# Performance work log

Hardware: AMD Instinct MI355X
Metric: run time of the kernel (lower is better)

The kernel has to match this reference:

```python
import jax, jax.numpy as jnp
import numpy as np

FEA_DIM = 256
NUM_HEADS = 8
B, N = 32, 48


def setup_inputs() -> dict:
    key = jax.random.key(0)
    ks = jax.random.split(key, 30)
    d = FEA_DIM
    inp = {
        "async_fea": jax.random.normal(ks[0], (B, N, d), dtype=jnp.float32),
        "sync_fea": jax.random.normal(ks[1], (B, N, d), dtype=jnp.float32),
        "async_adj": jax.random.randint(ks[2], (B, N, N), 0, 2, dtype=jnp.int32),
        "sync_adj": jax.random.randint(ks[3], (B, N, N), 0, 2, dtype=jnp.int32),
    }
    i = 4
    for pref in ("a_", "s_"):
        for nm in ("Wq", "Wk", "Wv", "Wo", "Wm"):
            inp[pref + nm] = 0.02 * jax.random.normal(ks[i], (d, d), dtype=jnp.float32); i += 1
            inp[pref + nm.replace("W", "b")] = 0.02 * jax.random.normal(ks[i], (d,), dtype=jnp.float32); i += 1
    return inp


def _aggregate(x_src, adj, fallback, Wq, bq, Wk, bk, Wv, bv, Wo, bo, Wm, bm):
    """For each target t: self-attention among neighbor set {s : adj[b,s,t] > 0}
    of x_src, mean-pool over neighbors, divide by count again, linear map.
    Targets with no neighbors fall back to `fallback`."""
    Bb, Nn, D = x_src.shape
    H = NUM_HEADS
    dh = D // H
    q = (x_src @ Wq.T + bq).reshape(Bb, Nn, H, dh)
    k = (x_src @ Wk.T + bk).reshape(Bb, Nn, H, dh)
    v = (x_src @ Wv.T + bv).reshape(Bb, Nn, H, dh)
    # shared pairwise scores among source nodes: [B, H, Q, K]
    scores = jnp.einsum("bqhd,bkhd->bhqk", q, k) / jnp.sqrt(jnp.float32(dh))
    # neighbor mask per target: adj[b, s, t] > 0 -> m[b, t, s]
    m = jnp.transpose(adj > 0, (0, 2, 1))  # [B, T, S] bool
    # per-target masked softmax over keys: logits [B, T, H, Q, K]
    key_bias = jnp.where(m[:, :, None, None, :], 0.0, -1e9)
    attn = jax.nn.softmax(scores[:, None] + key_bias, axis=-1)  # [B,T,H,Q,K]
    out = jnp.einsum("bthqk,bkhd->bthqd", attn, v).reshape(Bb, Nn, Nn, D)  # [B,T,Q,D]
    out = out @ Wo.T + bo
    mf = m.astype(out.dtype)  # [B, T, Q]
    cnt = mf.sum(-1)  # [B, T]
    denom = jnp.maximum(cnt, 1.0)
    # torch: mean over valid queries, then / edge_cnt  => sum / cnt^2
    pooled = jnp.einsum("btq,btqd->btd", mf, out) / (denom * denom)[..., None]
    mapped = pooled @ Wm.T + bm
    return jnp.where((cnt > 0)[..., None], mapped, fallback)


def reference(async_fea, sync_fea, async_adj, sync_adj,
              a_Wq, a_bq, a_Wk, a_bk, a_Wv, a_bv, a_Wo, a_bo, a_Wm, a_bm,
              s_Wq, s_bq, s_Wk, s_bk, s_Wv, s_bv, s_Wo, s_bo, s_Wm, s_bm):
    refined_async = _aggregate(sync_fea, sync_adj, async_fea,
                               a_Wq, a_bq, a_Wk, a_bk, a_Wv, a_bv, a_Wo, a_bo, a_Wm, a_bm)
    refined_sync = _aggregate(async_fea, async_adj, sync_fea,
                              s_Wq, s_bq, s_Wk, s_bk, s_Wv, s_bv, s_Wo, s_bo, s_Wm, s_bm)
    return jnp.concatenate([refined_async, refined_sync, async_fea, sync_fea], axis=2)
```

## Files before the change

### kernel.cpp

```cpp
#include <hip/hip_runtime.h>

typedef __attribute__((ext_vector_type(8))) short short8v;
typedef __attribute__((ext_vector_type(4))) float f32x4;

#define XPAD 264
#define ESTR 52

__device__ __forceinline__ unsigned short f2bf(float f) {
    union { float f; unsigned u; } v; v.f = f;
    unsigned u = v.u;
    return (unsigned short)((u + 0x7FFFu + ((u >> 16) & 1u)) >> 16);
}
__device__ __forceinline__ float bf2f(unsigned short u) {
    union { unsigned u; float f; } v; v.u = ((unsigned)u) << 16; return v.f;
}
__device__ __forceinline__ short8v cvt8(const float* p) {
    float4 lo = *(const float4*)p;
    float4 hi = *(const float4*)(p + 4);
    union { uint4 u; short8v s; } r;
    asm("v_cvt_pk_bf16_f32 %0, %1, %2" : "=v"(r.u.x) : "v"(lo.x), "v"(lo.y));
    asm("v_cvt_pk_bf16_f32 %0, %1, %2" : "=v"(r.u.y) : "v"(lo.z), "v"(lo.w));
    asm("v_cvt_pk_bf16_f32 %0, %1, %2" : "=v"(r.u.z) : "v"(hi.x), "v"(hi.y));
    asm("v_cvt_pk_bf16_f32 %0, %1, %2" : "=v"(r.u.w) : "v"(hi.z), "v"(hi.w));
    return r.s;
}

struct AggParams {
    const float *async_fea, *sync_fea;
    const int *async_adj, *sync_adj;
    const float *aWq, *abq, *aWk, *abk, *aWv, *abv, *aWo, *abo, *aWm, *abm;
    const float *sWq, *sbq, *sWk, *sbk, *sWv, *sbv, *sWo, *sbo, *sWm, *sbm;
    float *out;
};

__global__ __launch_bounds__(512) void block_kernel(AggParams p)
{
    __shared__ __attribute__((aligned(16))) char sm[118336];
    unsigned short* E_l  = (unsigned short*)(sm);
    unsigned short* Xb   = (unsigned short*)(sm);
    unsigned short* Qb   = (unsigned short*)(sm + 39936);
    float*          invd = (float*)(sm + 39936);
    unsigned short* Kb   = (unsigned short*)(sm + 65280);
    unsigned short* yv   = (unsigned short*)(sm + 65280);
    unsigned short* P_l  = (unsigned short*)(sm + 74592);
    unsigned short* Vb   = (unsigned short*)(sm + 90624);
    unsigned short* pool_l = (unsigned short*)(sm + 90624);
    float* msk   = (float*)(sm + 115968);
    float* cnt_l = (float*)(sm + 118272);

    const int bid = blockIdx.x, tid = threadIdx.x;
    const int agg = bid >> 7, rem = bid & 127;
    const int b = rem >> 2, tg = rem & 3;
    const int wave = tid >> 6, lane = tid & 63;
    const int l15 = lane & 15, g = lane >> 4;
    const int row_base = b * 48 + tg * 12;

    const float* Xsrc = agg ? p.async_fea : p.sync_fea;
    const float* fb   = agg ? p.sync_fea  : p.async_fea;
    const int*   adj  = agg ? p.async_adj : p.sync_adj;

    #pragma unroll
    for (int l = 0; l < 3; ++l) {
        int idx = l * 4096 + tid * 8;
        int row = idx >> 8, col = idx & 255;
        short8v v = cvt8(Xsrc + (b * 48 + row) * 256 + col);
        *(short8v*)(Xb + row * XPAD + col) = v;
    }
    for (int e = tid; e < 576; e += 512) {
        int tt = e / 48, s = e % 48;
        msk[tt * 48 + s] = (adj[(b * 48 + s) * 48 + tg * 12 + tt] > 0) ? 1.f : 0.f;
    }
    {
        const float4* fb4 = (const float4*)fb;
        float4* out4 = (float4*)p.out;
        for (int e = tid; e < 768; e += 512) {
            int r = e >> 6, c = e & 63;
            out4[(row_base + r) * 256 + 128 + agg * 64 + c] =
                fb4[(row_base + r) * 64 + c];
        }
    }
    __syncthreads();
    if (tid < 12) {
        float c = 0.f;
        for (int s = 0; s < 48; ++s) c += msk[tid * 48 + s];
        cnt_l[tid] = c;
    }

    for (int job = wave; job < 48; job += 8) {
        int mat = job >> 4;
        int cm = (job & 15) * 16;
        const float* W; const float* bias;
        if (agg == 0) {
            W    = (mat == 0) ? p.aWq : (mat == 1) ? p.aWk : p.aWv;
            bias = (mat == 0) ? p.abq : (mat == 1) ? p.abk : p.abv;
        } else {
            W    = (mat == 0) ? p.sWq : (mat == 1) ? p.sWk : p.sWv;
            bias = (mat == 0) ? p.sbq : (mat == 1) ? p.sbk : p.sbv;
        }
        const float* Wp = W + (cm + l15) * 256 + g * 8;
        f32x4 acc[3] = {{0,0,0,0},{0,0,0,0},{0,0,0,0}};
        #pragma unroll
        for (int kk = 0; kk < 8; ++kk) {
            short8v bf = cvt8(Wp + kk * 32);
            #pragma unroll
            for (int rt = 0; rt < 3; ++rt) {
                short8v a = *(const short8v*)(Xb + (rt * 16 + l15) * XPAD + kk * 32 + g * 8);
                acc[rt] = __builtin_amdgcn_mfma_f32_16x16x32_bf16(a, bf, acc[rt], 0, 0, 0);
            }
        }
        float bv = bias[cm + l15];
        unsigned short* dst = (mat == 0) ? Qb : (mat == 1) ? Kb : Vb;
        #pragma unroll
        for (int rt = 0; rt < 3; ++rt)
            #pragma unroll
            for (int i = 0; i < 4; ++i) {
                int row = rt * 16 + g * 4 + i;
                dst[row * XPAD + cm + l15] = f2bf(acc[rt][i] + bv);
            }
    }
    __syncthreads();

    const float scale = 0.17677669529663687f;
    #pragma unroll
    for (int jj = 0; jj < 3; ++jj) {
        int job = wave * 3 + jj;
        int h = job / 3, qt = job % 3;
        short8v a = *(const short8v*)(Qb + (qt * 16 + l15) * XPAD + h * 32 + g * 8);
        f32x4 acc[3];
        #pragma unroll
        for (int kt = 0; kt < 3; ++kt) {
            short8v kb = *(const short8v*)(Kb + (kt * 16 + l15) * XPAD + h * 32 + g * 8);
            f32x4 z = {0.f, 0.f, 0.f, 0.f};
            acc[kt] = __builtin_amdgcn_mfma_f32_16x16x32_bf16(a, kb, z, 0, 0, 0);
        }
        float sc[3][4], rm[4];
        #pragma unroll
        for (int i = 0; i < 4; ++i) {
            #pragma unroll
            for (int kt = 0; kt < 3; ++kt) sc[kt][i] = acc[kt][i] * scale;
            rm[i] = fmaxf(fmaxf(sc[0][i], sc[1][i]), sc[2][i]);
        }
        #pragma unroll
        for (int m = 1; m <= 8; m <<= 1)
            #pragma unroll
            for (int i = 0; i < 4; ++i) rm[i] = fmaxf(rm[i], __shfl_xor(rm[i], m));
        #pragma unroll
        for (int kt = 0; kt < 3; ++kt)
            #pragma unroll
            for (int i = 0; i < 4; ++i)
                E_l[(h * 48 + qt * 16 + g * 4 + i) * ESTR + kt * 16 + l15] =
                    f2bf(__expf(sc[kt][i] - rm[i]));
    }
    __syncthreads();

    if (tid < 384) {
        float erow[48];
        const uint2* er = (const uint2*)(E_l + tid * ESTR);
        #pragma unroll
        for (int v = 0; v < 12; ++v) {
            uint2 u = er[v];
            erow[v * 4 + 0] = bf2f((unsigned short)(u.x & 0xFFFF));
            erow[v * 4 + 1] = bf2f((unsigned short)(u.x >> 16));
            erow[v * 4 + 2] = bf2f((unsigned short)(u.y & 0xFFFF));
            erow[v * 4 + 3] = bf2f((unsigned short)(u.y >> 16));
        }
        int q = tid % 48;
        #pragma unroll
        for (int tt = 0; tt < 12; ++tt) {
            const float4* m4p = (const float4*)&msk[tt * 48];
            float ss = 0.f;
            #pragma unroll
            for (int k4 = 0; k4 < 12; ++k4) {
                float4 m4 = m4p[k4];
                ss += m4.x * erow[4 * k4] + m4.y * erow[4 * k4 + 1]
                    + m4.z * erow[4 * k4 + 2] + m4.w * erow[4 * k4 + 3];
            }
            invd[tt * 384 + tid] = (msk[tt * 48 + q] > 0.f) ? (1.f / ss) : 0.f;
        }
    }
    __syncthreads();

    if (tid < 384) {
        int h2 = tid / 48, k = tid % 48;
        float ecol[48];
        #pragma unroll
        for (int q = 0; q < 48; ++q) ecol[q] = bf2f(E_l[(h2 * 48 + q) * ESTR + k]);
        #pragma unroll
        for (int tt = 0; tt < 12; ++tt) {
            const float4* iv4 = (const float4*)&invd[tt * 384 + h2 * 48];
            float ss = 0.f;
            #pragma unroll
            for (int q4 = 0; q4 < 12; ++q4) {
                float4 v = iv4[q4];
                ss += v.x * ecol[4 * q4] + v.y * ecol[4 * q4 + 1]
                    + v.z * ecol[4 * q4 + 2] + v.w * ecol[4 * q4 + 3];
            }
            yv[tt * 388 + tid] = f2bf(msk[tt * 48 + k] * ss);
        }
    }
    __syncthreads();

    for (int e = tid; e < 1024; e += 512) {
        if (e < 768) {
            int tt = e >> 6, d4 = e & 63;
            const unsigned short* yr = yv + tt * 388 + (d4 >> 3) * 48;
            float px = 0.f, py = 0.f, pz = 0.f, pw = 0.f;
            #pragma unroll
            for (int k = 0; k < 48; ++k) {
                float yval = bf2f(yr[k]);
                uint2 vv = *(const uint2*)(Vb + k * XPAD + d4 * 4);
                px += yval * bf2f((unsigned short)(vv.x & 0xFFFF));
                py += yval * bf2f((unsigned short)(vv.x >> 16));
                pz += yval * bf2f((unsigned short)(vv.y & 0xFFFF));
                pw += yval * bf2f((unsigned short)(vv.y >> 16));
            }
            uint2 pk;
            pk.x = (unsigned)f2bf(px) | ((unsigned)f2bf(py) << 16);
            pk.y = (unsigned)f2bf(pz) | ((unsigned)f2bf(pw) << 16);
            *(uint2*)(P_l + tt * 264 + d4 * 4) = pk;
        } else {
            int e2 = e - 768;
            int tt = 12 + (e2 >> 6), d4 = e2 & 63;
            uint2 z; z.x = 0u; z.y = 0u;
            *(uint2*)(P_l + tt * 264 + d4 * 4) = z;
        }
    }
    __syncthreads();

    {
        const float* Wo = agg ? p.sWo : p.aWo;
        const float* bo = agg ? p.sbo : p.abo;
        for (int ct = wave; ct < 16; ct += 8) {
            f32x4 acc = {0.f, 0.f, 0.f, 0.f};
            const float* Wp = Wo + (ct * 16 + l15) * 256 + g * 8;
            #pragma unroll
            for (int kk = 0; kk < 8; ++kk) {
                short8v a = *(const short8v*)(P_l + l15 * 264 + kk * 32 + g * 8);
                short8v bf = cvt8(Wp + kk * 32);
                acc = __builtin_amdgcn_mfma_f32_16x16x32_bf16(a, bf, acc, 0, 0, 0);
            }
            int c = ct * 16 + l15;
            float bov = bo[c];
            #pragma unroll
            for (int i = 0; i < 4; ++i) {
                int t = g * 4 + i;
                float val = 0.f;
                if (t < 12) {
                    float cn = cnt_l[t];
                    float i1 = (cn > 0.f) ? 1.f / cn : 0.f;
                    val = acc[i] * i1 * i1 + bov * i1;
                }
                pool_l[t * 264 + c] = f2bf(val);
            }
        }
    }
    __syncthreads();

    {
        const float* Wm = agg ? p.sWm : p.aWm;
        const float* bm = agg ? p.sbm : p.abm;
        for (int ct = wave; ct < 16; ct += 8) {
            f32x4 acc = {0.f, 0.f, 0.f, 0.f};
            const float* Wp = Wm + (ct * 16 + l15) * 256 + g * 8;
            #pragma unroll
            for (int kk = 0; kk < 8; ++kk) {
                short8v a = *(const short8v*)(pool_l + l15 * 264 + kk * 32 + g * 8);
                short8v bf = cvt8(Wp + kk * 32);
                acc = __builtin_amdgcn_mfma_f32_16x16x32_bf16(a, bf, acc, 0, 0, 0);
            }
            int c = ct * 16 + l15;
            float bmv = bm[c];
            #pragma unroll
            for (int i = 0; i < 4; ++i) {
                int t = g * 4 + i;
                if (t < 12) {
                    int grow = row_base + t;
                    float cn = cnt_l[t];
                    float val = (cn > 0.f) ? (acc[i] + bmv) : fb[grow * 256 + c];
                    p.out[grow * 1024 + agg * 256 + c] = val;
                }
            }
        }
    }
}

extern "C" void kernel_launch(void* const* d_in, const int* in_sizes, int n_in,
                              void* d_out, int out_size, void* d_ws, size_t ws_size,
                              hipStream_t stream)
{
    AggParams p;
    p.async_fea = (const float*)d_in[0];
    p.sync_fea  = (const float*)d_in[1];
    p.async_adj = (const int*)d_in[2];
    p.sync_adj  = (const int*)d_in[3];
    p.aWq = (const float*)d_in[4];   p.abq = (const float*)d_in[5];
    p.aWk = (const float*)d_in[6];   p.abk = (const float*)d_in[7];
    p.aWv = (const float*)d_in[8];   p.abv = (const float*)d_in[9];
    p.aWo = (const float*)d_in[10];  p.abo = (const float*)d_in[11];
    p.aWm = (const float*)d_in[12];  p.abm = (const float*)d_in[13];
    p.sWq = (const float*)d_in[14];  p.sbq = (const float*)d_in[15];
    p.sWk = (const float*)d_in[16];  p.sbk = (const float*)d_in[17];
    p.sWv = (const float*)d_in[18];  p.sbv = (const float*)d_in[19];
    p.sWo = (const float*)d_in[20];  p.sbo = (const float*)d_in[21];
    p.sWm = (const float*)d_in[22];  p.sbm = (const float*)d_in[23];
    p.out = (float*)d_out;

    block_kernel<<<256, 512, 0, stream>>>(p);
}
```

Baseline: 60.00 us.

## Move masked-softmax denominators and attention pooling onto bf16 MFMA

Replaces the three scalar stages (per-target softmax denominators, inverse-weighted column sums, and the y·V pooling) with small 16x16x32 bf16 MFMA tiles. To support this it stores E both row-major and transposed, keeps V transposed, and packs the mask as bf16 with padded stride. The goal is to cut the long scalar FMA loops and the per-thread register arrays. In exchange it uses more LDS (about 159KB), which lowers occupancy, and it adds bf16 rounding to the mask-weighted sums.

```diff
diff --git a/kernel.cpp b/kernel.cpp
--- a/kernel.cpp
+++ b/kernel.cpp
@@ -2,16 +2,31 @@
 
 typedef __attribute__((ext_vector_type(8))) short short8v;
 typedef __attribute__((ext_vector_type(4))) float f32x4;
-
-#define XPAD 264
-#define ESTR 52
-
-__device__ __forceinline__ unsigned short f2bf(float f) {
+typedef unsigned short u16t;
+
+#define XP 264
+#define SP 52
+
+#define E_OFF    0
+#define ET_OFF   39936
+#define QB_OFF   79872
+#define KB_OFF   105216
+#define VT_OFF   130560
+#define MSK_OFF  157184
+#define CNT_OFF  158848
+#define SM_SIZE  158912
+#define XB_OFF   E_OFF
+#define IV_OFF   QB_OFF
+#define PL_OFF   (QB_OFF + 13312)
+#define YV_OFF   KB_OFF
+#define PO_OFF   (KB_OFF + 13312)
+
+__device__ __forceinline__ u16t f2bf(float f) {
     union { float f; unsigned u; } v; v.f = f;
     unsigned u = v.u;
-    return (unsigned short)((u + 0x7FFFu + ((u >> 16) & 1u)) >> 16);
-}
-__device__ __forceinline__ float bf2f(unsigned short u) {
+    return (u16t)((u + 0x7FFFu + ((u >> 16) & 1u)) >> 16);
+}
+__device__ __forceinline__ float bf2f(u16t u) {
     union { unsigned u; float f; } v; v.u = ((unsigned)u) << 16; return v.f;
 }
 __device__ __forceinline__ short8v cvt8(const float* p) {
@@ -24,6 +39,12 @@
     asm("v_cvt_pk_bf16_f32 %0, %1, %2" : "=v"(r.u.w) : "v"(hi.z), "v"(hi.w));
     return r.s;
 }
+__device__ __forceinline__ short8v ld52(const u16t* p) {
+    union { uint2 u[2]; short8v s; } r;
+    r.u[0] = *(const uint2*)(p);
+    r.u[1] = *(const uint2*)(p + 4);
+    return r.s;
+}
 
 struct AggParams {
     const float *async_fea, *sync_fea;
@@ -35,18 +56,19 @@
 
 __global__ __launch_bounds__(512) void block_kernel(AggParams p)
 {
-    __shared__ __attribute__((aligned(16))) char sm[118336];
-    unsigned short* E_l  = (unsigned short*)(sm);
-    unsigned short* Xb   = (unsigned short*)(sm);
-    unsigned short* Qb   = (unsigned short*)(sm + 39936);
-    float*          invd = (float*)(sm + 39936);
-    unsigned short* Kb   = (unsigned short*)(sm + 65280);
-    unsigned short* yv   = (unsigned short*)(sm + 65280);
-    unsigned short* P_l  = (unsigned short*)(sm + 74592);
-    unsigned short* Vb   = (unsigned short*)(sm + 90624);
-    unsigned short* pool_l = (unsigned short*)(sm + 90624);
-    float* msk   = (float*)(sm + 115968);
-    float* cnt_l = (float*)(sm + 118272);
+    __shared__ __attribute__((aligned(16))) char sm[SM_SIZE];
+    u16t* E_   = (u16t*)(sm + E_OFF);
+    u16t* ET_  = (u16t*)(sm + ET_OFF);
+    u16t* Xb   = (u16t*)(sm + XB_OFF);
+    u16t* Qb   = (u16t*)(sm + QB_OFF);
+    u16t* Kb   = (u16t*)(sm + KB_OFF);
+    u16t* VT   = (u16t*)(sm + VT_OFF);
+    u16t* mskb = (u16t*)(sm + MSK_OFF);
+    u16t* iv_  = (u16t*)(sm + IV_OFF);
+    u16t* yv_  = (u16t*)(sm + YV_OFF);
+    u16t* P_l  = (u16t*)(sm + PL_OFF);
+    u16t* po_  = (u16t*)(sm + PO_OFF);
+    float* cnt_l = (float*)(sm + CNT_OFF);
 
     const int bid = blockIdx.x, tid = threadIdx.x;
     const int agg = bid >> 7, rem = bid & 127;
@@ -63,12 +85,14 @@
     for (int l = 0; l < 3; ++l) {
         int idx = l * 4096 + tid * 8;
         int row = idx >> 8, col = idx & 255;
-        short8v v = cvt8(Xsrc + (b * 48 + row) * 256 + col);
-        *(short8v*)(Xb + row * XPAD + col) = v;
-    }
-    for (int e = tid; e < 576; e += 512) {
-        int tt = e / 48, s = e % 48;
-        msk[tt * 48 + s] = (adj[(b * 48 + s) * 48 + tg * 12 + tt] > 0) ? 1.f : 0.f;
+        *(short8v*)(Xb + row * XP + col) = cvt8(Xsrc + (b * 48 + row) * 256 + col);
+    }
+    for (int e = tid; e < 16 * SP; e += 512) {
+        int tt = e / SP, k = e - tt * SP;
+        u16t v = 0;
+        if (tt < 12 && k < 48)
+            v = (adj[(b * 48 + k) * 48 + tg * 12 + tt] > 0) ? (u16t)0x3F80 : (u16t)0;
+        mskb[e] = v;
     }
     {
         const float4* fb4 = (const float4*)fb;
@@ -82,7 +106,7 @@
     __syncthreads();
     if (tid < 12) {
         float c = 0.f;
-        for (int s = 0; s < 48; ++s) c += msk[tid * 48 + s];
+        for (int s = 0; s < 48; ++s) c += bf2f(mskb[tid * SP + s]);
         cnt_l[tid] = c;
     }
 
@@ -104,19 +128,25 @@
             short8v bf = cvt8(Wp + kk * 32);
             #pragma unroll
             for (int rt = 0; rt < 3; ++rt) {
-                short8v a = *(const short8v*)(Xb + (rt * 16 + l15) * XPAD + kk * 32 + g * 8);
+                short8v a = *(const short8v*)(Xb + (rt * 16 + l15) * XP + kk * 32 + g * 8);
                 acc[rt] = __builtin_amdgcn_mfma_f32_16x16x32_bf16(a, bf, acc[rt], 0, 0, 0);
             }
         }
         float bv = bias[cm + l15];
-        unsigned short* dst = (mat == 0) ? Qb : (mat == 1) ? Kb : Vb;
-        #pragma unroll
-        for (int rt = 0; rt < 3; ++rt)
-            #pragma unroll
-            for (int i = 0; i < 4; ++i) {
-                int row = rt * 16 + g * 4 + i;
-                dst[row * XPAD + cm + l15] = f2bf(acc[rt][i] + bv);
-            }
+        if (mat < 2) {
+            u16t* dst = (mat == 0) ? Qb : Kb;
+            #pragma unroll
+            for (int rt = 0; rt < 3; ++rt)
+                #pragma unroll
+                for (int i = 0; i < 4; ++i)
+                    dst[(rt * 16 + g * 4 + i) * XP + cm + l15] = f2bf(acc[rt][i] + bv);
+        } else {
+            #pragma unroll
+            for (int rt = 0; rt < 3; ++rt)
+                #pragma unroll
+                for (int i = 0; i < 4; ++i)
+                    VT[(cm + l15) * SP + rt * 16 + g * 4 + i] = f2bf(acc[rt][i] + bv);
+        }
     }
     __syncthreads();
 
@@ -125,11 +155,11 @@
     for (int jj = 0; jj < 3; ++jj) {
         int job = wave * 3 + jj;
         int h = job / 3, qt = job % 3;
-        short8v a = *(const short8v*)(Qb + (qt * 16 + l15) * XPAD + h * 32 + g * 8);
+        short8v a = *(const short8v*)(Qb + (qt * 16 + l15) * XP + h * 32 + g * 8);
         f32x4 acc[3];
         #pragma unroll
         for (int kt = 0; kt < 3; ++kt) {
-            short8v kb = *(const short8v*)(Kb + (kt * 16 + l15) * XPAD + h * 32 + g * 8);
+            short8v kb = *(const short8v*)(Kb + (kt * 16 + l15) * XP + h * 32 + g * 8);
             f32x4 z = {0.f, 0.f, 0.f, 0.f};
             acc[kt] = __builtin_amdgcn_mfma_f32_16x16x32_bf16(a, kb, z, 0, 0, 0);
         }
@@ -147,95 +177,87 @@
         #pragma unroll
         for (int kt = 0; kt < 3; ++kt)
             #pragma unroll
-            for (int i = 0; i < 4; ++i)
-                E_l[(h * 48 + qt * 16 + g * 4 + i) * ESTR + kt * 16 + l15] =
-                    f2bf(__expf(sc[kt][i] - rm[i]));
-    }
-    __syncthreads();
-
-    if (tid < 384) {
-        float erow[48];
-        const uint2* er = (const uint2*)(E_l + tid * ESTR);
-        #pragma unroll
-        for (int v = 0; v < 12; ++v) {
-            uint2 u = er[v];
-            erow[v * 4 + 0] = bf2f((unsigned short)(u.x & 0xFFFF));
-            erow[v * 4 + 1] = bf2f((unsigned short)(u.x >> 16));
-            erow[v * 4 + 2] = bf2f((unsigned short)(u.y & 0xFFFF));
-            erow[v * 4 + 3] = bf2f((unsigned short)(u.y >> 16));
-        }
-        int q = tid % 48;
-        #pragma unroll
-        for (int tt = 0; tt < 12; ++tt) {
-            const float4* m4p = (const float4*)&msk[tt * 48];
-            float ss = 0.f;
-            #pragma unroll
-            for (int k4 = 0; k4 < 12; ++k4) {
-                float4 m4 = m4p[k4];
-                ss += m4.x * erow[4 * k4] + m4.y * erow[4 * k4 + 1]
-                    + m4.z * erow[4 * k4 + 2] + m4.w * erow[4 * k4 + 3];
-            }
-            invd[tt * 384 + tid] = (msk[tt * 48 + q] > 0.f) ? (1.f / ss) : 0.f;
-        }
-    }
-    __syncthreads();
-
-    if (tid < 384) {
-        int h2 = tid / 48, k = tid % 48;
-        float ecol[48];
-        #pragma unroll
-        for (int q = 0; q < 48; ++q) ecol[q] = bf2f(E_l[(h2 * 48 + q) * ESTR + k]);
-        #pragma unroll
-        for (int tt = 0; tt < 12; ++tt) {
-            const float4* iv4 = (const float4*)&invd[tt * 384 + h2 * 48];
-            float ss = 0.f;
-            #pragma unroll
-            for (int q4 = 0; q4 < 12; ++q4) {
-                float4 v = iv4[q4];
-                ss += v.x * ecol[4 * q4] + v.y * ecol[4 * q4 + 1]
-                    + v.z * ecol[4 * q4 + 2] + v.w * ecol[4 * q4 + 3];
-            }
-            yv[tt * 388 + tid] = f2bf(msk[tt * 48 + k] * ss);
-        }
-    }
-    __syncthreads();
-
-    for (int e = tid; e < 1024; e += 512) {
-        if (e < 768) {
-            int tt = e >> 6, d4 = e & 63;
-            const unsigned short* yr = yv + tt * 388 + (d4 >> 3) * 48;
-            float px = 0.f, py = 0.f, pz = 0.f, pw = 0.f;
-            #pragma unroll
-            for (int k = 0; k < 48; ++k) {
-                float yval = bf2f(yr[k]);
-                uint2 vv = *(const uint2*)(Vb + k * XPAD + d4 * 4);
-                px += yval * bf2f((unsigned short)(vv.x & 0xFFFF));
-                py += yval * bf2f((unsigned short)(vv.x >> 16));
-                pz += yval * bf2f((unsigned short)(vv.y & 0xFFFF));
-                pw += yval * bf2f((unsigned short)(vv.y >> 16));
-            }
-            uint2 pk;
-            pk.x = (unsigned)f2bf(px) | ((unsigned)f2bf(py) << 16);
-            pk.y = (unsigned)f2bf(pz) | ((unsigned)f2bf(pw) << 16);
-            *(uint2*)(P_l + tt * 264 + d4 * 4) = pk;
-        } else {
-            int e2 = e - 768;
-            int tt = 12 + (e2 >> 6), d4 = e2 & 63;
-            uint2 z; z.x = 0u; z.y = 0u;
-            *(uint2*)(P_l + tt * 264 + d4 * 4) = z;
-        }
+            for (int i = 0; i < 4; ++i) {
+                u16t ev = f2bf(__expf(sc[kt][i] - rm[i]));
+                int q = qt * 16 + g * 4 + i, k = kt * 16 + l15;
+                E_[(h * 48 + q) * SP + k] = ev;
+                ET_[(h * 48 + k) * SP + q] = ev;
+            }
+    }
+    __syncthreads();
+
+    #pragma unroll
+    for (int jj = 0; jj < 3; ++jj) {
+        int rt = wave * 3 + jj;
+        const u16t* Arow = E_ + (rt * 16 + l15) * SP;
+        const u16t* Brow = mskb + l15 * SP;
+        f32x4 acc = {0.f, 0.f, 0.f, 0.f};
+        short8v a0 = ld52(Arow + g * 8), b0 = ld52(Brow + g * 8);
+        acc = __builtin_amdgcn_mfma_f32_16x16x32_bf16(a0, b0, acc, 0, 0, 0);
+        short8v a1 = {0,0,0,0,0,0,0,0}, b1 = {0,0,0,0,0,0,0,0};
+        if (g < 2) { a1 = ld52(Arow + 32 + g * 8); b1 = ld52(Brow + 32 + g * 8); }
+        acc = __builtin_amdgcn_mfma_f32_16x16x32_bf16(a1, b1, acc, 0, 0, 0);
+        #pragma unroll
+        for (int i = 0; i < 4; ++i) {
+            int row = rt * 16 + g * 4 + i;
+            int h = row / 48, q = row - h * 48;
+            float mq = bf2f(mskb[l15 * SP + q]);
+            float ivv = (mq > 0.f) ? (1.f / acc[i]) : 0.f;
+            iv_[(h * 16 + l15) * SP + q] = f2bf(ivv);
+        }
+    }
+    __syncthreads();
+
+    #pragma unroll
+    for (int jj = 0; jj < 3; ++jj) {
+        int job = wave * 3 + jj;
+        int h = job / 3, kt = job % 3;
+        const u16t* Arow = iv_ + (h * 16 + l15) * SP;
+        const u16t* Brow = ET_ + (h * 48 + kt * 16 + l15) * SP;
+        f32x4 acc = {0.f, 0.f, 0.f, 0.f};
+        short8v a0 = ld52(Arow + g * 8), b0 = ld52(Brow + g * 8);
+        acc = __builtin_amdgcn_mfma_f32_16x16x32_bf16(a0, b0, acc, 0, 0, 0);
+        short8v a1 = {0,0,0,0,0,0,0,0}, b1 = {0,0,0,0,0,0,0,0};
+        if (g < 2) { a1 = ld52(Arow + 32 + g * 8); b1 = ld52(Brow + 32 + g * 8); }
+        acc = __builtin_amdgcn_mfma_f32_16x16x32_bf16(a1, b1, acc, 0, 0, 0);
+        #pragma unroll
+        for (int i = 0; i < 4; ++i) {
+            int tt = g * 4 + i, k = kt * 16 + l15;
+            float mk = bf2f(mskb[tt * SP + k]);
+            yv_[(h * 16 + tt) * SP + k] = f2bf(acc[i] * mk);
+        }
+    }
+    __syncthreads();
+
+    #pragma unroll
+    for (int jj = 0; jj < 2; ++jj) {
+        int job = wave * 2 + jj;
+        int h = job >> 1, dt = job & 1;
+        const u16t* Arow = yv_ + (h * 16 + l15) * SP;
+        const u16t* Brow = VT + (h * 32 + dt * 16 + l15) * SP;
+        f32x4 acc = {0.f, 0.f, 0.f, 0.f};
+        short8v a0 = ld52(Arow + g * 8), b0 = ld52(Brow + g * 8);
+        acc = __builtin_amdgcn_mfma_f32_16x16x32_bf16(a0, b0, acc, 0, 0, 0);
+        short8v a1 = {0,0,0,0,0,0,0,0}, b1 = {0,0,0,0,0,0,0,0};
+        if (g < 2) { a1 = ld52(Arow + 32 + g * 8); b1 = ld52(Brow + 32 + g * 8); }
+        acc = __builtin_amdgcn_mfma_f32_16x16x32_bf16(a1, b1, acc, 0, 0, 0);
+        #pragma unroll
+        for (int i = 0; i < 4; ++i)
+            P_l[(g * 4 + i) * XP + h * 32 + dt * 16 + l15] = f2bf(acc[i]);
     }
     __syncthreads();
 
     {
         const float* Wo = agg ? p.sWo : p.aWo;
         const float* bo = agg ? p.sbo : p.abo;
-        for (int ct = wave; ct < 16; ct += 8) {
+        #pragma unroll
+        for (int jj = 0; jj < 2; ++jj) {
+            int ct = wave * 2 + jj;
             f32x4 acc = {0.f, 0.f, 0.f, 0.f};
             const float* Wp = Wo + (ct * 16 + l15) * 256 + g * 8;
             #pragma unroll
             for (int kk = 0; kk < 8; ++kk) {
-                short8v a = *(const short8v*)(P_l + l15 * 264 + kk * 32 + g * 8);
+                short8v a = *(const short8v*)(P_l + l15 * XP + kk * 32 + g * 8);
                 short8v bf = cvt8(Wp + kk * 32);
                 acc = __builtin_amdgcn_mfma_f32_16x16x32_bf16(a, bf, acc, 0, 0, 0);
             }
@@ -250,7 +272,7 @@
                     float i1 = (cn > 0.f) ? 1.f / cn : 0.f;
                     val = acc[i] * i1 * i1 + bov * i1;
                 }
-                pool_l[t * 264 + c] = f2bf(val);
+                po_[t * XP + c] = f2bf(val);
             }
         }
     }
@@ -259,12 +281,14 @@
     {
         const float* Wm = agg ? p.sWm : p.aWm;
         const float* bm = agg ? p.sbm : p.abm;
-        for (int ct = wave; ct < 16; ct += 8) {
+        #pragma unroll
+        for (int jj = 0; jj < 2; ++jj) {
+            int ct = wave * 2 + jj;
             f32x4 acc = {0.f, 0.f, 0.f, 0.f};
             const float* Wp = Wm + (ct * 16 + l15) * 256 + g * 8;
             #pragma unroll
             for (int kk = 0; kk < 8; ++kk) {
-                short8v a = *(const short8v*)(pool_l + l15 * 264 + kk * 32 + g * 8);
+                short8v a = *(const short8v*)(po_ + l15 * XP + kk * 32 + g * 8);
                 short8v bf = cvt8(Wp + kk * 32);
                 acc = __builtin_amdgcn_mfma_f32_16x16x32_bf16(a, bf, acc, 0, 0, 0);
             }
```

New measurement: 53.98 us. -10.0%, faster.
